# Optimization experiments

Hardware: AMD Instinct MI355X
Metric: run time of the kernel (lower is better)

The kernel has to match this reference:

```python
import jax, jax.numpy as jnp
import numpy as np

TEMP = 0.07
LN_EPS = 1e-5


def _l2norm(x, eps=1e-12):
    n = jnp.linalg.norm(x, axis=-1, keepdims=True)
    return x / jnp.maximum(n, eps)


def setup_inputs() -> dict:
    key = jax.random.key(0)
    ks = jax.random.split(key, 8)
    B, N, D, S = 1024, 100000, 1024, 2
    scale = 1.0 / np.sqrt(D)
    return {
        "q": jax.random.normal(ks[0], (B, D), jnp.float32),
        "bank_values": jax.random.normal(ks[1], (N, D), jnp.float32),
        "proj_w": jax.random.normal(ks[2], (S, D, D), jnp.float32) * scale,
        "proj_b": jax.random.normal(ks[3], (S, D), jnp.float32) * 0.01,
        "unify_w": jax.random.normal(ks[4], (S, D, D), jnp.float32) * scale,
        "unify_b": jax.random.normal(ks[5], (S, D), jnp.float32) * 0.01,
        "ln_gamma": jnp.ones((D,), jnp.float32),
        "ln_beta": jnp.zeros((D,), jnp.float32),
        "top_m": 32,
    }


def reference(q, bank_values, proj_w, proj_b, unify_w, unify_b, ln_gamma, ln_beta, top_m):
    # PrototypeBank.build: keys = L2-normalized values (detached)
    keys = _l2norm(bank_values)  # [N, D]
    num_scales = proj_w.shape[0]
    ref = jnp.zeros_like(q)
    for s in range(num_scales):  # small fixed structural loop
        p = q @ proj_w[s].T + proj_b[s]                       # [B, D] Linear
        scores = _l2norm(p) @ keys.T                          # [B, N] cosine
        top_s, top_i = jax.lax.top_k(scores, top_m)           # [B, m]
        attn = jax.nn.softmax(top_s / TEMP, axis=-1)          # [B, m]
        z = jnp.einsum('bm,bmd->bd', attn, bank_values[top_i])  # weighted gather-sum
        ref = ref + z @ unify_w[s].T + unify_b[s]
    mu = ref.mean(axis=-1, keepdims=True)
    var = ref.var(axis=-1, keepdims=True)
    out = (ref - mu) * jax.lax.rsqrt(var + LN_EPS) * ln_gamma + ln_beta
    return out
```

## Files before the change

### kernel.cpp

```cpp
#include <hip/hip_runtime.h>
#include <math.h>


static inline size_t align256(size_t x){ return (x + 255) & ~size_t(255); }

typedef short bf16x8 __attribute__((ext_vector_type(8)));
typedef float f32x4  __attribute__((ext_vector_type(4)));

#define GLOAD_LDS16(gp, lp) \
  __builtin_amdgcn_global_load_lds((const __attribute__((address_space(1))) unsigned int*)(gp), \
                                   (__attribute__((address_space(3))) unsigned int*)(lp), 16, 0, 0)

__device__ inline unsigned short f2bf(float f){
  unsigned int u = __float_as_uint(f);
  u += 0x7fffu + ((u >> 16) & 1u);
  return (unsigned short)(u >> 16);
}
__device__ inline float bf2f(unsigned int h16){
  return __uint_as_float(h16 << 16);
}

__global__ __launch_bounds__(256) void row_rnorm_kernel(
    const float* __restrict__ X, float* __restrict__ rn, int rows, int D)
{
  int wv = threadIdx.x >> 6, lane = threadIdx.x & 63;
  int r = blockIdx.x * 4 + wv;
  if (r >= rows) return;
  const float4* xr = (const float4*)(X + (size_t)r * D);
  int nv = D >> 2;
  float ss = 0.f;
  for (int i = lane; i < nv; i += 64){
    float4 v = xr[i];
    ss = fmaf(v.x,v.x, fmaf(v.y,v.y, fmaf(v.z,v.z, fmaf(v.w,v.w, ss))));
  }
  #pragma unroll
  for (int off = 32; off; off >>= 1) ss += __shfl_xor(ss, off);
  if (lane == 0) rn[r] = 1.f / fmaxf(sqrtf(ss), 1e-12f);
}

__global__ __launch_bounds__(256) void convert_bf16_kernel(
    const float* __restrict__ X, const float* __restrict__ rowscale,
    unsigned short* __restrict__ out, long total8, int D)
{
  long i = (long)blockIdx.x * 256 + threadIdx.x;
  const long stride = (long)gridDim.x * 256;
  for (; i < total8; i += stride){
    long e = i * 8;
    int r = (int)(e / D);
    float sc = rowscale ? rowscale[r] : 1.f;
    float4 v0 = *(const float4*)(X + e);
    float4 v1 = *(const float4*)(X + e + 4);
    v0.x*=sc; v0.y*=sc; v0.z*=sc; v0.w*=sc;
    v1.x*=sc; v1.y*=sc; v1.z*=sc; v1.w*=sc;
    uint4 w;
    w.x = (unsigned)f2bf(v0.x) | ((unsigned)f2bf(v0.y) << 16);
    w.y = (unsigned)f2bf(v0.z) | ((unsigned)f2bf(v0.w) << 16);
    w.z = (unsigned)f2bf(v1.x) | ((unsigned)f2bf(v1.y) << 16);
    w.w = (unsigned)f2bf(v1.z) | ((unsigned)f2bf(v1.w) << 16);
    *(uint4*)(out + e) = w;
  }
}

template<int RM, int RN, bool ACCUM>
__global__ __launch_bounds__(256) void gemm_nt_kernel(
    const float* __restrict__ A, const float* __restrict__ B,
    const float* __restrict__ bias, const float* __restrict__ bscale,
    float* __restrict__ C, int M, int Nn, int K, int Brows, int ldc)
{
  __shared__ float As[16][RM*64 + 4];
  __shared__ float Bs[16][RN*64 + 4];
  const int t  = threadIdx.x;
  const int tm = t >> 4, tn = t & 15;
  const int m0 = blockIdx.y * (RM*64), n0 = blockIdx.x * (RN*64);

  float acc[RM][RN][4][4];
  #pragma unroll
  for (int r=0;r<RM;++r)
    #pragma unroll
    for (int c=0;c<RN;++c)
      #pragma unroll
      for (int i=0;i<4;++i)
        #pragma unroll
        for (int j=0;j<4;++j) acc[r][c][i][j]=0.f;

  for (int kp = 0; kp < K; kp += 16){
    #pragma unroll
    for (int l = 0; l < RM; ++l){
      int li = t + l*256;
      int row = li >> 2, kq = (li & 3) << 2;
      float4 v = *(const float4*)(A + (size_t)(m0+row)*K + kp + kq);
      As[kq+0][row]=v.x; As[kq+1][row]=v.y; As[kq+2][row]=v.z; As[kq+3][row]=v.w;
    }
    #pragma unroll
    for (int l = 0; l < RN; ++l){
      int li = t + l*256;
      int row = li >> 2, kq = (li & 3) << 2;
      int gn = n0 + row;
      float4 v = make_float4(0.f,0.f,0.f,0.f);
      float sc = 1.f;
      if (gn < Brows){
        v = *(const float4*)(B + (size_t)gn*K + kp + kq);
        if (bscale) sc = bscale[gn];
      }
      Bs[kq+0][row]=v.x*sc; Bs[kq+1][row]=v.y*sc; Bs[kq+2][row]=v.z*sc; Bs[kq+3][row]=v.w*sc;
    }
    __syncthreads();
    #pragma unroll
    for (int kk = 0; kk < 16; ++kk){
      float av[RM][4], bv[RN][4];
      #pragma unroll
      for (int r=0;r<RM;++r){
        float4 a = *(const float4*)&As[kk][r*64 + tm*4];
        av[r][0]=a.x; av[r][1]=a.y; av[r][2]=a.z; av[r][3]=a.w;
      }
      #pragma unroll
      for (int c=0;c<RN;++c){
        float4 b = *(const float4*)&Bs[kk][c*64 + tn*4];
        bv[c][0]=b.x; bv[c][1]=b.y; bv[c][2]=b.z; bv[c][3]=b.w;
      }
      #pragma unroll
      for (int r=0;r<RM;++r)
        #pragma unroll
        for (int c=0;c<RN;++c)
          #pragma unroll
          for (int i=0;i<4;++i)
            #pragma unroll
            for (int j=0;j<4;++j)
              acc[r][c][i][j] = fmaf(av[r][i], bv[c][j], acc[r][c][i][j]);
    }
    __syncthreads();
  }

  #pragma unroll
  for (int r=0;r<RM;++r){
    #pragma unroll
    for (int i=0;i<4;++i){
      int gm = m0 + r*64 + tm*4 + i;
      #pragma unroll
      for (int c=0;c<RN;++c){
        int gn = n0 + c*64 + tn*4;
        if (gn >= Nn) continue;
        float* cp = C + (size_t)gm*ldc + gn;
        float o0=acc[r][c][i][0], o1=acc[r][c][i][1], o2=acc[r][c][i][2], o3=acc[r][c][i][3];
        if (gn + 3 < Nn){
          float4 o = make_float4(o0,o1,o2,o3);
          if (bias){ float4 bb = *(const float4*)&bias[gn]; o.x+=bb.x; o.y+=bb.y; o.z+=bb.z; o.w+=bb.w; }
          if (ACCUM){ float4 cc = *(const float4*)cp; o.x+=cc.x; o.y+=cc.y; o.z+=cc.z; o.w+=cc.w; }
          *(float4*)cp = o;
        } else {
          float ov[4] = {o0,o1,o2,o3};
          for (int j=0;j<4;++j){
            if (gn + j < Nn){
              float o = ov[j];
              if (bias)  o += bias[gn+j];
              if (ACCUM) o += cp[j];
              cp[j] = o;
            }
          }
        }
      }
    }
  }
}

__global__ __launch_bounds__(256) void scores_mfma_kernel(
    const unsigned short* __restrict__ Abf, const unsigned short* __restrict__ Bbf,
    unsigned short* __restrict__ C, int M, int Nn, int K, int ldc)
{
  __shared__ __align__(16) unsigned char smem[16384];

  const int t = threadIdx.x;
  const int lane = t & 63, wid = t >> 6;
  const int wm = wid >> 1, wn = wid & 1;
  const int l15 = lane & 15, l4 = lane >> 4;
  const int m0 = blockIdx.x * 128, n0 = blockIdx.y * 128;

  f32x4 acc[4][4];
  #pragma unroll
  for (int i=0;i<4;++i)
    #pragma unroll
    for (int j=0;j<4;++j) acc[i][j] = (f32x4)0.f;

  const int srow = t >> 2;
  const int sb   = (t & 3) * 16;
  const int ldsb = wid * 1024;

  for (int kp = 0; kp < K; kp += 32){
    #pragma unroll
    for (int i = 0; i < 2; ++i){
      int row = srow + i*64;
      int src = sb ^ ((row & 3) << 4);
      const unsigned char* ga = (const unsigned char*)Abf
          + ((size_t)(m0+row)*K + kp)*2 + src;
      GLOAD_LDS16(ga, smem + i*4096 + ldsb);
      int gn = n0 + row; if (gn >= Nn) gn = Nn - 1;
      const unsigned char* gb = (const unsigned char*)Bbf
          + ((size_t)gn*K + kp)*2 + src;
      GLOAD_LDS16(gb, smem + 8192 + i*4096 + ldsb);
    }
    __syncthreads();

    const unsigned char* As_ = smem;
    const unsigned char* Bs_ = smem + 8192;
    bf16x8 Bf[4];
    #pragma unroll
    for (int fn = 0; fn < 4; ++fn){
      int br = wn*64 + fn*16 + l15;
      Bf[fn] = *(const bf16x8*)(Bs_ + br*64 + ((l4*16) ^ ((br & 3) << 4)));
    }
    #pragma unroll
    for (int fm = 0; fm < 4; ++fm){
      int ar = wm*64 + fm*16 + l15;
      bf16x8 Af = *(const bf16x8*)(As_ + ar*64 + ((l4*16) ^ ((ar & 3) << 4)));
      #pragma unroll
      for (int fn = 0; fn < 4; ++fn)
        acc[fm][fn] = __builtin_amdgcn_mfma_f32_16x16x32_bf16(Af, Bf[fn], acc[fm][fn], 0,0,0);
    }
    __syncthreads();
  }

  #pragma unroll
  for (int fm = 0; fm < 4; ++fm){
    int row = m0 + wm*64 + fm*16 + l4*4;
    #pragma unroll
    for (int fn = 0; fn < 4; ++fn){
      int col = n0 + wn*64 + fn*16 + l15;
      if (col < Nn){
        unsigned short* cp = C + (size_t)row*ldc + col;
        #pragma unroll
        for (int r = 0; r < 4; ++r) cp[(size_t)r*ldc] = f2bf(acc[fm][fn][r]);
      }
    }
  }
}

__global__ __launch_bounds__(256) void chunk_filter_kernel(
    const unsigned short* __restrict__ scores, int ldc, int colbase, int Nwindow,
    int NC, float* __restrict__ cand_s, int* __restrict__ cand_i,
    int chunk0, int nchunks_total, int cap, float eps)
{
  extern __shared__ float lds[];
  __shared__ float sv[256];
  __shared__ float tau_s;
  __shared__ int cnt;
  const int row = blockIdx.x, t = threadIdx.x;
  const int lc = blockIdx.y;
  const int col0l = lc * NC;
  int ncols = Nwindow - col0l; if (ncols > NC) ncols = NC;
  const int gchunk = chunk0 + lc;
  const unsigned short* sr = scores + (size_t)row * ldc + col0l;

  float m0 = -INFINITY, m1 = -INFINITY, m2 = -INFINITY, m3 = -INFINITY;
  const int nc8 = ncols >> 3;
  const uint4* sr8 = (const uint4*)sr;
  float4* lds4 = (float4*)lds;
  for (int j = t; j < nc8; j += 256){
    uint4 v = sr8[j];
    float4 a = make_float4(bf2f(v.x & 0xffffu), bf2f(v.x >> 16),
                           bf2f(v.y & 0xffffu), bf2f(v.y >> 16));
    float4 b = make_float4(bf2f(v.z & 0xffffu), bf2f(v.z >> 16),
                           bf2f(v.w & 0xffffu), bf2f(v.w >> 16));
    lds4[j*2]   = a;
    lds4[j*2+1] = b;
    m0 = fmaxf(m0, fmaxf(a.x, b.x)); m1 = fmaxf(m1, fmaxf(a.y, b.y));
    m2 = fmaxf(m2, fmaxf(a.z, b.z)); m3 = fmaxf(m3, fmaxf(a.w, b.w));
  }
  for (int j = (nc8 << 3) + t; j < ncols; j += 256){
    float v = bf2f((unsigned)sr[j]);
    lds[j] = v;
    m0 = fmaxf(m0, v);
  }
  sv[t] = fmaxf(fmaxf(m0, m1), fmaxf(m2, m3));
  __syncthreads();

  for (int k = 2; k <= 256; k <<= 1){
    for (int j = k >> 1; j > 0; j >>= 1){
      int p = t ^ j;
      float a = sv[t], b = sv[p];
      bool up = ((t & k) == 0);
      float keep = (t < p) ? (up ? fmaxf(a,b) : fminf(a,b))
                           : (up ? fminf(a,b) : fmaxf(a,b));
      __syncthreads();
      sv[t] = keep;
      __syncthreads();
    }
  }
  if (t == 0){ tau_s = sv[31]; cnt = 0; }
  __syncthreads();
  const float thr = tau_s - eps;

  float* cs = cand_s + ((size_t)row * nchunks_total + gchunk) * cap;
  int*   ci = cand_i + ((size_t)row * nchunks_total + gchunk) * cap;

  for (int j = t; j < ncols; j += 256){
    float v = lds[j];
    if (v >= thr){
      int pos = atomicAdd(&cnt, 1);
      if (pos < cap){ cs[pos] = v; ci[pos] = colbase + col0l + j; }
    }
  }
  __syncthreads();
  int n = cnt < cap ? cnt : cap;
  for (int j = n + t; j < cap; j += 256) ci[j] = -1;
}

__global__ __launch_bounds__(256) void select_softmax_gather_kernel(
    const float* __restrict__ cand_s, const int* __restrict__ cand_i,
    const float* __restrict__ p, const float* __restrict__ rn_bank,
    const float* __restrict__ pnorm, const float* __restrict__ bank,
    float* __restrict__ z, int ncap, int D, int topm, float invtemp, float eps)
{
  __shared__ float p_s[1024];
  __shared__ float vs[1024]; __shared__ int vi[1024];
  __shared__ float sv[256];
  __shared__ int   cidx[256];
  __shared__ float rv[256];
  __shared__ float tau_s;
  __shared__ int cnt;
  const int row = blockIdx.x, t = threadIdx.x;
  const int lane = t & 63, wid = t >> 6;

  const float4* pr = (const float4*)(p + (size_t)row * D);
  for (int i = t; i < (D >> 2); i += 256) ((float4*)p_s)[i] = pr[i];
  const float* cs = cand_s + (size_t)row * ncap;
  const int*  ci = cand_i + (size_t)row * ncap;
  for (int j = t; j < ncap; j += 256){
    int k = ci[j];
    vi[j] = k;
    vs[j] = (k >= 0) ? cs[j] : -INFINITY;
  }
  __syncthreads();

  float m = -INFINITY;
  for (int j = t; j < ncap; j += 256) m = fmaxf(m, vs[j]);
  sv[t] = m;
  __syncthreads();
  for (int k = 2; k <= 256; k <<= 1){
    for (int j = k >> 1; j > 0; j >>= 1){
      int pp = t ^ j;
      float a = sv[t], b = sv[pp];
      bool up = ((t & k) == 0);
      float keep = (t < pp) ? (up ? fmaxf(a,b) : fminf(a,b))
                            : (up ? fminf(a,b) : fmaxf(a,b));
      __syncthreads();
      sv[t] = keep;
      __syncthreads();
    }
  }
  if (t == 0){ tau_s = sv[31]; cnt = 0; }
  __syncthreads();
  const float thr = tau_s - eps;

  for (int j = t; j < ncap; j += 256){
    if (vi[j] >= 0 && vs[j] >= thr){
      int pos = atomicAdd(&cnt, 1);
      if (pos < 256) cidx[pos] = vi[j];
    }
  }
  __syncthreads();
  const int n2 = cnt < 256 ? cnt : 256;
  rv[t] = -INFINITY;
  if (t >= n2) cidx[t] = 0x7fffffff;
  __syncthreads();

  const int nj = D >> 8;
  for (int c = wid; c < n2; c += 4){
    int idx = cidx[c];
    const float4* kr = (const float4*)(bank + (size_t)idx * D);
    float ss = 0.f;
    for (int j = 0; j < nj; ++j){
      float4 kv = kr[lane + j*64];
      float4 pv = *(const float4*)&p_s[(lane + j*64) << 2];
      ss = fmaf(pv.x,kv.x, fmaf(pv.y,kv.y, fmaf(pv.z,kv.z, fmaf(pv.w,kv.w, ss))));
    }
    #pragma unroll
    for (int off = 32; off; off >>= 1) ss += __shfl_xor(ss, off);
    if (lane == 0) rv[c] = ss * rn_bank[idx];
  }
  __syncthreads();

  for (int k = 2; k <= 256; k <<= 1){
    for (int j = k >> 1; j > 0; j >>= 1){
      int pp = t ^ j;
      float av = rv[t];  int ai = cidx[t];
      float bv = rv[pp]; int bi = cidx[pp];
      bool up = ((t & k) == 0);
      bool agtb = (av > bv) || (av == bv && ai < bi);
      bool keepA = (t < pp) ? (up ? agtb : !agtb)
                            : (up ? !agtb : agtb);
      __syncthreads();
      if (keepA){ rv[t] = av; cidx[t] = ai; } else { rv[t] = bv; cidx[t] = bi; }
      __syncthreads();
    }
  }

  if (t == 0){
    float pn = pnorm[row] * invtemp;
    float mx = rv[0] * pn;
    float sum = 0.f;
    for (int i = 0; i < topm; ++i){
      float w = expf(rv[i]*pn - mx);
      sv[i] = w; sum += w;
    }
    float inv = 1.f / sum;
    for (int i = 0; i < topm; ++i) sv[i] *= inv;
  }
  __syncthreads();

  for (int d4 = t; d4 < (D >> 2); d4 += 256){
    float ax=0.f, ay=0.f, az=0.f, aw=0.f;
    for (int i = 0; i < topm; ++i){
      float a = sv[i];
      const float4 v = *(const float4*)(bank + (size_t)cidx[i]*D + (d4<<2));
      ax = fmaf(a, v.x, ax); ay = fmaf(a, v.y, ay);
      az = fmaf(a, v.z, az); aw = fmaf(a, v.w, aw);
    }
    *(float4*)(z + (size_t)row*D + (d4<<2)) = make_float4(ax,ay,az,aw);
  }
}

__global__ __launch_bounds__(256) void layernorm_kernel(
    const float* __restrict__ ref, const float* __restrict__ gamma,
    const float* __restrict__ beta, float* __restrict__ out, int D, float eps)
{
  __shared__ float s1[4], s2[4];
  const int row = blockIdx.x, t = threadIdx.x;
  const float4* xr = (const float4*)(ref + (size_t)row*D);
  int nv = D >> 2;
  float sum = 0.f, ssq = 0.f;
  for (int i = t; i < nv; i += 256){
    float4 v = xr[i];
    sum += v.x+v.y+v.z+v.w;
    ssq = fmaf(v.x,v.x, fmaf(v.y,v.y, fmaf(v.z,v.z, fmaf(v.w,v.w, ssq))));
  }
  const int lane = t & 63, wid = t >> 6;
  #pragma unroll
  for (int off = 32; off; off >>= 1){ sum += __shfl_xor(sum, off); ssq += __shfl_xor(ssq, off); }
  if (lane == 0){ s1[wid] = sum; s2[wid] = ssq; }
  __syncthreads();
  sum = s1[0]+s1[1]+s1[2]+s1[3];
  ssq = s2[0]+s2[1]+s2[2]+s2[3];
  float mu  = sum / (float)D;
  float var = ssq / (float)D - mu*mu;
  float rs  = rsqrtf(var + eps);
  const float4* g4 = (const float4*)gamma;
  const float4* b4 = (const float4*)beta;
  float4* o4 = (float4*)(out + (size_t)row*D);
  for (int i = t; i < nv; i += 256){
    float4 v = xr[i], g = g4[i], bb = b4[i];
    float4 o;
    o.x = (v.x-mu)*rs*g.x + bb.x;
    o.y = (v.y-mu)*rs*g.y + bb.y;
    o.z = (v.z-mu)*rs*g.z + bb.z;
    o.w = (v.w-mu)*rs*g.w + bb.w;
    o4[i] = o;
  }
}

extern "C" void kernel_launch(void* const* d_in, const int* in_sizes, int n_in,
                              void* d_out, int out_size, void* d_ws, size_t ws_size,
                              hipStream_t stream)
{
  const float* q       = (const float*)d_in[0];
  const float* bank    = (const float*)d_in[1];
  const float* proj_w  = (const float*)d_in[2];
  const float* proj_b  = (const float*)d_in[3];
  const float* unify_w = (const float*)d_in[4];
  const float* unify_b = (const float*)d_in[5];
  const float* gamma   = (const float*)d_in[6];
  const float* beta    = (const float*)d_in[7];

  const int D = in_sizes[6];
  const int B = in_sizes[0] / D;
  const int N = in_sizes[1] / D;
  const int S = in_sizes[2] / (D * D);
  const int R = S * B;
  const int TOPM = 32;
  const int CAP  = 64;
  const int NC   = 12544;
  const int WCH  = 4;
  const float INVTEMP = 1.0f / 0.07f;
  const float EPS = 0.025f;

  const int NCH = (N + NC - 1) / NC;
  const int SCW = NC * WCH;

  char* wsb = (char*)d_ws;
  size_t off = 0;
  auto take = [&](size_t bytes)->char*{ char* p = wsb + off; off += align256(bytes); return p; };
  float* rn_bank = (float*)take((size_t)N*4);
  float* pnorm   = (float*)take((size_t)R*4);
  float* p       = (float*)take((size_t)R*D*4);
  float* z       = (float*)take((size_t)R*D*4);
  float* ref     = (float*)take((size_t)B*D*4);
  float* cand_s  = (float*)take((size_t)R*NCH*CAP*4);
  int*   cand_i  = (int*)  take((size_t)R*NCH*CAP*4);
  unsigned short* bank_bf = (unsigned short*)take((size_t)N*D*2);
  unsigned short* p_bf    = (unsigned short*)take((size_t)R*D*2);
  unsigned short* scores  = (unsigned short*)take((size_t)R*(size_t)SCW*2);

  row_rnorm_kernel<<<(N+3)/4, 256, 0, stream>>>(bank, rn_bank, N, D);
  convert_bf16_kernel<<<2048, 256, 0, stream>>>(
      bank, rn_bank, bank_bf, (long)N*D/8, D);

  dim3 g1(D/64, B/64);
  for (int s = 0; s < S; ++s)
    gemm_nt_kernel<1,1,false><<<g1, 256, 0, stream>>>(
        q, proj_w + (size_t)s*D*D, proj_b + (size_t)s*D, nullptr,
        p + (size_t)s*B*D, B, D, D, D, D);

  row_rnorm_kernel<<<(R+3)/4, 256, 0, stream>>>(p, pnorm, R, D);
  convert_bf16_kernel<<<1024, 256, 0, stream>>>(
      p, nullptr, p_bf, (long)R*D/8, D);

  for (int w0 = 0; w0 < N; w0 += SCW){
    int nw = N - w0; if (nw > SCW) nw = SCW;
    dim3 g2(R/128, (nw + 127)/128);
    scores_mfma_kernel<<<g2, 256, 0, stream>>>(
        p_bf, bank_bf + (size_t)w0*D,
        scores, R, nw, D, SCW);
    int ncw = (nw + NC - 1) / NC;
    chunk_filter_kernel<<<dim3(R, ncw), 256, (size_t)NC*4, stream>>>(
        scores, SCW, w0, nw, NC, cand_s, cand_i,
        w0 / NC, NCH, CAP, EPS);
  }

  select_softmax_gather_kernel<<<R, 256, 0, stream>>>(
      cand_s, cand_i, p, rn_bank, pnorm, bank, z,
      NCH*CAP, D, TOPM, INVTEMP, EPS);

  for (int s = 0; s < S; ++s){
    if (s == 0)
      gemm_nt_kernel<1,1,false><<<g1, 256, 0, stream>>>(
          z + (size_t)s*B*D, unify_w + (size_t)s*D*D, unify_b + (size_t)s*D, nullptr,
          ref, B, D, D, D, D);
    else
      gemm_nt_kernel<1,1,true><<<g1, 256, 0, stream>>>(
          z + (size_t)s*B*D, unify_w + (size_t)s*D*D, unify_b + (size_t)s*D, nullptr,
          ref, B, D, D, D, D);
  }

  layernorm_kernel<<<B, 256, 0, stream>>>(ref, gamma, beta, (float*)d_out, D, 1e-5f);
}
```

Baseline: 1.512 ms.

## Double K-step per LDS stage in scores GEMM and launch over full bank at once

The scores MFMA kernel now stages a 64-wide K slice per iteration, with a 128-byte row stride and an 8-way XOR swizzle, and issues two MFMAs per fragment pair. This halves the number of barriers and loop iterations. The host drops the windowed loop over the bank and runs a single scores GEMM plus a single chunk filter over all N columns. That removes launch overhead and tail effects, but the score buffer grows to R×N bf16, which no longer fits in cache between the two kernels and raises memory traffic and workspace size.

After: 1.429 ms. -5.4%, faster.

```diff
diff --git a/kernel.cpp b/kernel.cpp
--- a/kernel.cpp
+++ b/kernel.cpp
@@ -167,7 +167,7 @@
     const unsigned short* __restrict__ Abf, const unsigned short* __restrict__ Bbf,
     unsigned short* __restrict__ C, int M, int Nn, int K, int ldc)
 {
-  __shared__ __align__(16) unsigned char smem[16384];
+  __shared__ __align__(16) unsigned char smem[32768];
 
   const int t = threadIdx.x;
   const int lane = t & 63, wid = t >> 6;
@@ -181,40 +181,48 @@
     #pragma unroll
     for (int j=0;j<4;++j) acc[i][j] = (f32x4)0.f;
 
-  const int srow = t >> 2;
-  const int sb   = (t & 3) * 16;
+  const int srow = t >> 3;
+  const int sb   = (t & 7) * 16;
   const int ldsb = wid * 1024;
 
-  for (int kp = 0; kp < K; kp += 32){
-    #pragma unroll
-    for (int i = 0; i < 2; ++i){
-      int row = srow + i*64;
-      int src = sb ^ ((row & 3) << 4);
+  for (int kp = 0; kp < K; kp += 64){
+    #pragma unroll
+    for (int i = 0; i < 4; ++i){
+      int row = srow + i*32;
+      int src = sb ^ ((row & 7) << 4);
       const unsigned char* ga = (const unsigned char*)Abf
           + ((size_t)(m0+row)*K + kp)*2 + src;
       GLOAD_LDS16(ga, smem + i*4096 + ldsb);
       int gn = n0 + row; if (gn >= Nn) gn = Nn - 1;
       const unsigned char* gb = (const unsigned char*)Bbf
           + ((size_t)gn*K + kp)*2 + src;
-      GLOAD_LDS16(gb, smem + 8192 + i*4096 + ldsb);
+      GLOAD_LDS16(gb, smem + 16384 + i*4096 + ldsb);
     }
     __syncthreads();
 
     const unsigned char* As_ = smem;
-    const unsigned char* Bs_ = smem + 8192;
-    bf16x8 Bf[4];
+    const unsigned char* Bs_ = smem + 16384;
+    bf16x8 B0[4], B1[4];
     #pragma unroll
     for (int fn = 0; fn < 4; ++fn){
       int br = wn*64 + fn*16 + l15;
-      Bf[fn] = *(const bf16x8*)(Bs_ + br*64 + ((l4*16) ^ ((br & 3) << 4)));
+      int xr = (br & 7) << 4;
+      const unsigned char* bp = Bs_ + br*128;
+      B0[fn] = *(const bf16x8*)(bp + (( l4*16      ) ^ xr));
+      B1[fn] = *(const bf16x8*)(bp + ((64 + l4*16 ) ^ xr));
     }
     #pragma unroll
     for (int fm = 0; fm < 4; ++fm){
       int ar = wm*64 + fm*16 + l15;
-      bf16x8 Af = *(const bf16x8*)(As_ + ar*64 + ((l4*16) ^ ((ar & 3) << 4)));
+      int xr = (ar & 7) << 4;
+      const unsigned char* ap = As_ + ar*128;
+      bf16x8 A0 = *(const bf16x8*)(ap + (( l4*16      ) ^ xr));
+      bf16x8 A1 = *(const bf16x8*)(ap + ((64 + l4*16 ) ^ xr));
       #pragma unroll
-      for (int fn = 0; fn < 4; ++fn)
-        acc[fm][fn] = __builtin_amdgcn_mfma_f32_16x16x32_bf16(Af, Bf[fn], acc[fm][fn], 0,0,0);
+      for (int fn = 0; fn < 4; ++fn){
+        acc[fm][fn] = __builtin_amdgcn_mfma_f32_16x16x32_bf16(A0, B0[fn], acc[fm][fn], 0,0,0);
+        acc[fm][fn] = __builtin_amdgcn_mfma_f32_16x16x32_bf16(A1, B1[fn], acc[fm][fn], 0,0,0);
+      }
     }
     __syncthreads();
   }
@@ -478,12 +486,10 @@
   const int TOPM = 32;
   const int CAP  = 64;
   const int NC   = 12544;
-  const int WCH  = 4;
   const float INVTEMP = 1.0f / 0.07f;
   const float EPS = 0.025f;
 
   const int NCH = (N + NC - 1) / NC;
-  const int SCW = NC * WCH;
 
   char* wsb = (char*)d_ws;
   size_t off = 0;
@@ -497,7 +503,7 @@
   int*   cand_i  = (int*)  take((size_t)R*NCH*CAP*4);
   unsigned short* bank_bf = (unsigned short*)take((size_t)N*D*2);
   unsigned short* p_bf    = (unsigned short*)take((size_t)R*D*2);
-  unsigned short* scores  = (unsigned short*)take((size_t)R*(size_t)SCW*2);
+  unsigned short* scores  = (unsigned short*)take((size_t)R*(size_t)N*2);
 
   row_rnorm_kernel<<<(N+3)/4, 256, 0, stream>>>(bank, rn_bank, N, D);
   convert_bf16_kernel<<<2048, 256, 0, stream>>>(
@@ -513,16 +519,13 @@
   convert_bf16_kernel<<<1024, 256, 0, stream>>>(
       p, nullptr, p_bf, (long)R*D/8, D);
 
-  for (int w0 = 0; w0 < N; w0 += SCW){
-    int nw = N - w0; if (nw > SCW) nw = SCW;
-    dim3 g2(R/128, (nw + 127)/128);
+  {
+    dim3 g2(R/128, (N + 127)/128);
     scores_mfma_kernel<<<g2, 256, 0, stream>>>(
-        p_bf, bank_bf + (size_t)w0*D,
-        scores, R, nw, D, SCW);
-    int ncw = (nw + NC - 1) / NC;
-    chunk_filter_kernel<<<dim3(R, ncw), 256, (size_t)NC*4, stream>>>(
-        scores, SCW, w0, nw, NC, cand_s, cand_i,
-        w0 / NC, NCH, CAP, EPS);
+        p_bf, bank_bf, scores, R, N, D, N);
+    chunk_filter_kernel<<<dim3(R, NCH), 256, (size_t)NC*4, stream>>>(
+        scores, N, 0, N, NC, cand_s, cand_i,
+        0, NCH, CAP, EPS);
   }
 
   select_softmax_gather_kernel<<<R, 256, 0, stream>>>(
```
